# Kernel tuning notes

Hardware: AMD Instinct MI355X
Metric: run time of the kernel (lower is better)

Reference implementation:

```python
import jax, jax.numpy as jnp
import numpy as np

N, D, K = 16384, 256, 4096   # tokens, feature dim, codebook_size
GAMMA = 0.99


def setup_inputs() -> dict:
    key = jax.random.key(0)
    k1, k2, k3 = jax.random.split(key, 3)
    features = jax.random.normal(k1, (N, D), dtype=jnp.float32)
    mask = jax.random.uniform(k2, (N,)) < 0.9
    codebook = jax.random.normal(k3, (K, D), dtype=jnp.float32)  # hk RandomNormal init
    count = jnp.zeros((K,), jnp.float32)
    avg = jnp.zeros((K,), jnp.float32)
    return {"features": features, "mask": mask, "codebook": codebook,
            "count": count, "avg": avg}


def reference(features, mask, codebook, count, avg):
    sg = jax.lax.stop_gradient
    prev_codebook = codebook

    # pairwise squared distances [N, K] via ||f||^2 - 2 f.C^T + ||c||^2
    f2 = jnp.sum(features * features, axis=-1)            # [N]
    c2 = jnp.sum(codebook * codebook, axis=-1)            # [K]
    distance = f2[:, None] - 2.0 * (features @ codebook.T) + c2[None, :]
    distance = jnp.where(mask[:, None], distance, jnp.inf)

    assign_fwd = jnp.argmin(distance, axis=1)             # [N] nearest code per token
    assign_rev = jnp.argmin(distance, axis=0)             # [K] nearest token per code
    features_fwd = codebook[assign_fwd]                   # [N, D]
    features_rev = features[assign_rev]                   # [K, D]

    # straight-through estimator
    out_features = sg(features_fwd) + features - sg(features)

    total = jnp.maximum(mask.sum(), 1).astype(features.dtype)
    commitment = jnp.mean((sg(features_fwd) - features) ** 2, axis=-1)
    commitment_loss = jnp.where(mask, commitment, 0.0).sum() / total

    # scatter-add assignment counts (masked) and feature sums (unmasked, as in source)
    assignment_count = jnp.zeros((K,), jnp.float32).at[assign_fwd].add(
        mask.astype(jnp.float32))
    assignment_mask = assignment_count < 1

    count = (1.0 - GAMMA) * assignment_count + GAMMA * count
    avg = (1.0 - GAMMA) * assignment_count / total + GAMMA * avg
    alpha = jnp.exp(-avg * K * 10.0 / (1.0 - GAMMA) - 0.001)

    feat_sum = jnp.zeros_like(codebook).at[assign_fwd].add(features)  # [K, D]
    assigned_update = (GAMMA * codebook + (1.0 - GAMMA) * feat_sum)
    assigned_update = assigned_update / jnp.maximum(count[:, None], 1.0)
    unassigned_update = (1.0 - alpha)[:, None] * codebook + alpha[:, None] * features_rev
    new_codebook = jnp.where(assignment_mask[:, None], assigned_update, unassigned_update)

    # pmean(delta) is identity on a single device; final = prev + (prev - new), as in source
    codebook_delta = prev_codebook - new_codebook
    new_codebook = prev_codebook + codebook_delta

    unassigned_percent = (assignment_count > 0).mean()
    return (out_features, assign_fwd, commitment_loss, unassigned_percent,
            count, avg, new_codebook)
```

## Files before the change

kernel.cpp:

```cpp
#include <hip/hip_runtime.h>
#include <math.h>

typedef unsigned long long u64;
typedef unsigned int u32;

#define N_TOK 16384
#define DIM   256
#define KCB   4096

#define WS_ROWMIN   0
#define WS_COLMIN   131072
#define WS_CNT      163840
#define WS_CPART    180224
#define WS_TOTAL    181248
#define WS_FLAG     181252
#define WS_F2       181312
#define WS_C2       246848
#define WS_END      263232

#define OUT_FEAT    0
#define OUT_ASSIGN  4194304
#define OUT_CLOSS   4210688
#define OUT_UPCT    4210689
#define OUT_COUNT   4210690
#define OUT_AVG     4214786
#define OUT_CB      4218882

#define C_1MG 0.009999999776482582f

__device__ __forceinline__ u32 fkey(float d) {
    u32 u = __float_as_uint(d);
    return (u & 0x80000000u) ? ~u : (u | 0x80000000u);
}
__device__ __forceinline__ u64 u64min(u64 a, u64 b) { return a < b ? a : b; }
__device__ __forceinline__ u64 shflxor64(u64 v, int m) {
    int lo = __shfl_xor((int)(u32)(v & 0xFFFFFFFFULL), m, 64);
    int hi = __shfl_xor((int)(u32)(v >> 32), m, 64);
    return ((u64)(u32)hi << 32) | (u32)lo;
}
__device__ __forceinline__ bool read_mask(const void* mp, int flag, int n) {
    if (flag == 2) return ((const float*)mp)[n] != 0.0f;
    if (flag == 1) return ((const int*)mp)[n] != 0;
    return ((const unsigned char*)mp)[n] != 0;
}

__global__ void k_detect(const void* __restrict__ mp, int* __restrict__ flag) {
    if (threadIdx.x == 0) {
        const u32* w = (const u32*)mp;
        bool allf = true, alli = true, any1 = false;
        for (int i = 0; i < 64; ++i) {
            u32 x = w[i];
            if (x != 0u && x != 0x3F800000u) allf = false;
            if (x == 0x3F800000u) any1 = true;
            if (x > 1u) alli = false;
        }
        *flag = (allf && any1) ? 2 : (alli ? 1 : 0);
    }
}

__global__ __launch_bounds__(256)
void k_norms(const float* __restrict__ F, const float* __restrict__ CB,
             const void* __restrict__ mp, const int* __restrict__ flagp,
             float* __restrict__ f2, float* __restrict__ c2) {
    __shared__ float red[4];
    const int b = blockIdx.x, d = threadIdx.x;
    const float* src = (b < N_TOK) ? (F + (size_t)b * DIM) : (CB + (size_t)(b - N_TOK) * DIM);
    float v = src[d];
    float s = v * v;
#pragma unroll
    for (int m = 32; m > 0; m >>= 1) s += __shfl_xor(s, m, 64);
    if ((d & 63) == 0) red[d >> 6] = s;
    __syncthreads();
    if (d == 0) {
        float tot = red[0] + red[1] + red[2] + red[3];
        if (b < N_TOK) {
            bool msk = read_mask(mp, *flagp, b);
            f2[b] = msk ? tot : __builtin_huge_valf();
        } else {
            c2[b - N_TOK] = tot;
        }
    }
}

__global__ __launch_bounds__(256, 2)
void k_gemm(const float* __restrict__ F, const float* __restrict__ CB,
            const float* __restrict__ f2, const float* __restrict__ c2,
            u64* __restrict__ rowmin, u64* __restrict__ colmin) {
    __shared__ float As[128][32];
    __shared__ float Bs[128][32];
    __shared__ u64 colred[4][128];

    const int t = threadIdx.x;
    const int ty = t >> 4, tx = t & 15;
    const int wave = t >> 6;
    const int rowbase = blockIdx.x * 128;
    const int kseg = blockIdx.y * 512;

    u64 rowbest[8];
#pragma unroll
    for (int i = 0; i < 8; ++i) rowbest[i] = ~0ULL;

    for (int c = 0; c < 4; ++c) {
        const int kbase = kseg + c * 128;
        float acc[8][8];
#pragma unroll
        for (int i = 0; i < 8; ++i)
#pragma unroll
            for (int j = 0; j < 8; ++j) acc[i][j] = 0.0f;

        for (int dc = 0; dc < 8; ++dc) {
            const int db = dc * 32;
#pragma unroll
            for (int i = 0; i < 4; ++i) {
                int g = t + i * 256;
                int r = g >> 3;
                int d4 = (g & 7) << 2;
                int dsw = d4 ^ (((r >> 3) & 7) << 2);
                float4 va = *(const float4*)(F + (size_t)(rowbase + r) * DIM + db + d4);
                *(float4*)&As[r][dsw] = va;
                float4 vb = *(const float4*)(CB + (size_t)(kbase + r) * DIM + db + d4);
                *(float4*)&Bs[r][dsw] = vb;
            }
            __syncthreads();
#pragma unroll
            for (int dd = 0; dd < 32; dd += 4) {
                float4 a[8], b[8];
#pragma unroll
                for (int i = 0; i < 8; ++i)
                    a[i] = *(const float4*)&As[ty * 8 + i][dd ^ ((ty & 7) << 2)];
#pragma unroll
                for (int j = 0; j < 8; ++j)
                    b[j] = *(const float4*)&Bs[tx * 8 + j][dd ^ ((tx & 7) << 2)];
#pragma unroll
                for (int i = 0; i < 8; ++i)
#pragma unroll
                    for (int j = 0; j < 8; ++j) {
                        acc[i][j] = fmaf(a[i].x, b[j].x, acc[i][j]);
                        acc[i][j] = fmaf(a[i].y, b[j].y, acc[i][j]);
                        acc[i][j] = fmaf(a[i].z, b[j].z, acc[i][j]);
                        acc[i][j] = fmaf(a[i].w, b[j].w, acc[i][j]);
                    }
            }
            __syncthreads();
        }

        float c2k[8], f2r[8];
#pragma unroll
        for (int j = 0; j < 8; ++j) c2k[j] = c2[kbase + tx * 8 + j];
#pragma unroll
        for (int i = 0; i < 8; ++i) f2r[i] = f2[rowbase + ty * 8 + i];
        u64 cbst[8];
#pragma unroll
        for (int j = 0; j < 8; ++j) cbst[j] = ~0ULL;
#pragma unroll
        for (int i = 0; i < 8; ++i) {
#pragma unroll
            for (int j = 0; j < 8; ++j) {
                float dist = (f2r[i] - 2.0f * acc[i][j]) + c2k[j];
                u64 hk = (u64)fkey(dist) << 32;
                rowbest[i] = u64min(rowbest[i], hk | (u32)(kbase + tx * 8 + j));
                cbst[j]    = u64min(cbst[j],    hk | (u32)(rowbase + ty * 8 + i));
            }
        }
#pragma unroll
        for (int j = 0; j < 8; ++j) {
            cbst[j] = u64min(cbst[j], shflxor64(cbst[j], 16));
            cbst[j] = u64min(cbst[j], shflxor64(cbst[j], 32));
        }
        if ((t & 63) < 16) {
#pragma unroll
            for (int j = 0; j < 8; ++j) colred[wave][tx * 8 + j] = cbst[j];
        }
        __syncthreads();
        if (t < 128) {
            u64 m = u64min(u64min(colred[0][t], colred[1][t]),
                           u64min(colred[2][t], colred[3][t]));
            atomicMin(&colmin[kbase + t], m);
        }
        __syncthreads();
    }

#pragma unroll
    for (int i = 0; i < 8; ++i) {
        u64 r = rowbest[i];
        r = u64min(r, shflxor64(r, 1));
        r = u64min(r, shflxor64(r, 2));
        r = u64min(r, shflxor64(r, 4));
        r = u64min(r, shflxor64(r, 8));
        if (tx == 0) atomicMin(&rowmin[rowbase + ty * 8 + i], r);
    }
}

__global__ __launch_bounds__(256)
void k_token(const float* __restrict__ F, const float* __restrict__ CB,
             const u64* __restrict__ rowmin, const void* __restrict__ mp,
             const int* __restrict__ flagp,
             float* __restrict__ out_feat, float* __restrict__ out_assign,
             float* __restrict__ cnt, float* __restrict__ fsum,
             float* __restrict__ cpart) {
    __shared__ float red[4];
    const int n = blockIdx.x, d = threadIdx.x;
    const int k = (int)(u32)(rowmin[n] & 0xFFFFFFFFULL);
    const float f = F[(size_t)n * DIM + d];
    const float cv = CB[(size_t)k * DIM + d];
    out_feat[(size_t)n * DIM + d] = (cv + f) - f;
    const float df = cv - f;
    float s = df * df;
#pragma unroll
    for (int m = 32; m > 0; m >>= 1) s += __shfl_xor(s, m, 64);
    if ((d & 63) == 0) red[d >> 6] = s;
    __syncthreads();
    atomicAdd(&fsum[(size_t)k * DIM + d], f);
    if (d == 0) {
        out_assign[n] = (float)k;
        bool msk = read_mask(mp, *flagp, n);
        if (msk) {
            float tot = red[0] + red[1] + red[2] + red[3];
            atomicAdd(&cnt[k], 1.0f);
            atomicAdd(&cpart[n & 255], tot * (1.0f / 256.0f));
        }
    }
}

__global__ __launch_bounds__(256)
void k_scalars(const float* __restrict__ cnt, const float* __restrict__ cpart,
               float* __restrict__ totf, float* __restrict__ out) {
    __shared__ float redf[4], redc[4];
    __shared__ int redi[4];
    const int t = threadIdx.x;
    float ts = 0.0f;
    int asg = 0;
    for (int i = t; i < KCB; i += 256) {
        float v = cnt[i];
        ts += v;
        asg += (v > 0.0f) ? 1 : 0;
    }
    float cs = cpart[t];
#pragma unroll
    for (int m = 32; m > 0; m >>= 1) {
        ts += __shfl_xor(ts, m, 64);
        cs += __shfl_xor(cs, m, 64);
        asg += __shfl_xor(asg, m, 64);
    }
    if ((t & 63) == 0) { redf[t >> 6] = ts; redc[t >> 6] = cs; redi[t >> 6] = asg; }
    __syncthreads();
    if (t == 0) {
        float total = redf[0] + redf[1] + redf[2] + redf[3];
        total = fmaxf(total, 1.0f);
        float closs = (redc[0] + redc[1] + redc[2] + redc[3]) / total;
        int a = redi[0] + redi[1] + redi[2] + redi[3];
        totf[0] = total;
        out[OUT_CLOSS] = closs;
        out[OUT_UPCT] = (float)a / 4096.0f;
    }
}

__global__ __launch_bounds__(256)
void k_cbupd(const float* __restrict__ F, const float* __restrict__ CB,
             const float* __restrict__ cnt_in, const float* __restrict__ avg_in,
             const float* __restrict__ ac_, const float* __restrict__ fsum,
             const u64* __restrict__ colmin, const float* __restrict__ totf,
             float* __restrict__ out_count, float* __restrict__ out_avg,
             float* __restrict__ out_cb) {
    const int k = blockIdx.x, d = threadIdx.x;
    const float ac = ac_[k];
    const float total = totf[0];
    const float cn = C_1MG * ac + 0.99f * cnt_in[k];
    const float av = (C_1MG * ac) / total + 0.99f * avg_in[k];
    const float arg = ((-av * 4096.0f) * 10.0f) / C_1MG - 0.001f;
    const float alpha = expf(arg);
    const int tok = (int)(u32)(colmin[k] & 0xFFFFFFFFULL);
    const float cb = CB[(size_t)k * DIM + d];
    const float fs = fsum[(size_t)k * DIM + d];
    const float fr = F[(size_t)tok * DIM + d];
    const float assigned = (0.99f * cb + C_1MG * fs) / fmaxf(cn, 1.0f);
    const float unass = (1.0f - alpha) * cb + alpha * fr;
    const float nc = (ac < 1.0f) ? assigned : unass;
    out_cb[(size_t)k * DIM + d] = cb + (cb - nc);
    if (d == 0) { out_count[k] = cn; out_avg[k] = av; }
}

extern "C" void kernel_launch(void* const* d_in, const int* in_sizes, int n_in,
                              void* d_out, int out_size, void* d_ws, size_t ws_size,
                              hipStream_t stream) {
    const float* F   = (const float*)d_in[0];
    const void*  Mp  = d_in[1];
    const float* CB  = (const float*)d_in[2];
    const float* CNT = (const float*)d_in[3];
    const float* AVG = (const float*)d_in[4];
    float* out = (float*)d_out;
    char* ws = (char*)d_ws;
    if (ws_size < (size_t)WS_END) return;

    u64*   rowmin = (u64*)(ws + WS_ROWMIN);
    u64*   colmin = (u64*)(ws + WS_COLMIN);
    float* cnt    = (float*)(ws + WS_CNT);
    float* cpart  = (float*)(ws + WS_CPART);
    float* totf   = (float*)(ws + WS_TOTAL);
    int*   flag   = (int*)(ws + WS_FLAG);
    float* f2     = (float*)(ws + WS_F2);
    float* c2     = (float*)(ws + WS_C2);
    float* fsum   = out + OUT_CB;

    hipMemsetAsync(ws, 0xFF, 163840, stream);
    hipMemsetAsync(ws + WS_CNT, 0, WS_FLAG - WS_CNT, stream);
    hipMemsetAsync(fsum, 0, (size_t)KCB * DIM * sizeof(float), stream);

    k_detect<<<1, 64, 0, stream>>>(Mp, flag);
    k_norms<<<N_TOK + KCB, 256, 0, stream>>>(F, CB, Mp, flag, f2, c2);
    k_gemm<<<dim3(128, 8), 256, 0, stream>>>(F, CB, f2, c2, rowmin, colmin);
    k_token<<<N_TOK, 256, 0, stream>>>(F, CB, rowmin, Mp, flag,
                                       out + OUT_FEAT, out + OUT_ASSIGN,
                                       cnt, fsum, cpart);
    k_scalars<<<1, 256, 0, stream>>>(cnt, cpart, totf, out);
    k_cbupd<<<KCB, 256, 0, stream>>>(F, CB, CNT, AVG, cnt, fsum, colmin, totf,
                                     out + OUT_COUNT, out + OUT_AVG, out + OUT_CB);
}
```

Measured before the change: 641.6 us.

## Split distance GEMM into finer K tiles and raise occupancy target

The distance GEMM now gives each block a single 128-code tile instead of looping over four tiles, which quadruples the grid. The launch bound moves from 2 to 4 blocks per CU, and LDS operand reads shrink from float4 to float2 to lower register pressure. Per-row minima are reduced and pushed with atomics inside the row loop rather than kept live across chunks. This aims for more waves in flight to hide latency, at the cost of four times as many rowmin atomics and possible spills under the tighter register cap.

Result: no change. 639.5 us (-0.3%).

```diff
diff --git a/kernel.cpp b/kernel.cpp
--- a/kernel.cpp
+++ b/kernel.cpp
@@ -82,7 +82,7 @@
     }
 }
 
-__global__ __launch_bounds__(256, 2)
+__global__ __launch_bounds__(256, 4)
 void k_gemm(const float* __restrict__ F, const float* __restrict__ CB,
             const float* __restrict__ f2, const float* __restrict__ c2,
             u64* __restrict__ rowmin, u64* __restrict__ colmin) {
@@ -94,100 +94,86 @@
     const int ty = t >> 4, tx = t & 15;
     const int wave = t >> 6;
     const int rowbase = blockIdx.x * 128;
-    const int kseg = blockIdx.y * 512;
-
-    u64 rowbest[8];
-#pragma unroll
-    for (int i = 0; i < 8; ++i) rowbest[i] = ~0ULL;
-
-    for (int c = 0; c < 4; ++c) {
-        const int kbase = kseg + c * 128;
-        float acc[8][8];
-#pragma unroll
-        for (int i = 0; i < 8; ++i)
-#pragma unroll
-            for (int j = 0; j < 8; ++j) acc[i][j] = 0.0f;
-
-        for (int dc = 0; dc < 8; ++dc) {
-            const int db = dc * 32;
-#pragma unroll
-            for (int i = 0; i < 4; ++i) {
-                int g = t + i * 256;
-                int r = g >> 3;
-                int d4 = (g & 7) << 2;
-                int dsw = d4 ^ (((r >> 3) & 7) << 2);
-                float4 va = *(const float4*)(F + (size_t)(rowbase + r) * DIM + db + d4);
-                *(float4*)&As[r][dsw] = va;
-                float4 vb = *(const float4*)(CB + (size_t)(kbase + r) * DIM + db + d4);
-                *(float4*)&Bs[r][dsw] = vb;
-            }
-            __syncthreads();
-#pragma unroll
-            for (int dd = 0; dd < 32; dd += 4) {
-                float4 a[8], b[8];
-#pragma unroll
-                for (int i = 0; i < 8; ++i)
-                    a[i] = *(const float4*)&As[ty * 8 + i][dd ^ ((ty & 7) << 2)];
-#pragma unroll
-                for (int j = 0; j < 8; ++j)
-                    b[j] = *(const float4*)&Bs[tx * 8 + j][dd ^ ((tx & 7) << 2)];
-#pragma unroll
-                for (int i = 0; i < 8; ++i)
-#pragma unroll
-                    for (int j = 0; j < 8; ++j) {
-                        acc[i][j] = fmaf(a[i].x, b[j].x, acc[i][j]);
-                        acc[i][j] = fmaf(a[i].y, b[j].y, acc[i][j]);
-                        acc[i][j] = fmaf(a[i].z, b[j].z, acc[i][j]);
-                        acc[i][j] = fmaf(a[i].w, b[j].w, acc[i][j]);
-                    }
-            }
-            __syncthreads();
-        }
-
-        float c2k[8], f2r[8];
-#pragma unroll
-        for (int j = 0; j < 8; ++j) c2k[j] = c2[kbase + tx * 8 + j];
-#pragma unroll
-        for (int i = 0; i < 8; ++i) f2r[i] = f2[rowbase + ty * 8 + i];
-        u64 cbst[8];
-#pragma unroll
-        for (int j = 0; j < 8; ++j) cbst[j] = ~0ULL;
-#pragma unroll
-        for (int i = 0; i < 8; ++i) {
-#pragma unroll
-            for (int j = 0; j < 8; ++j) {
-                float dist = (f2r[i] - 2.0f * acc[i][j]) + c2k[j];
-                u64 hk = (u64)fkey(dist) << 32;
-                rowbest[i] = u64min(rowbest[i], hk | (u32)(kbase + tx * 8 + j));
-                cbst[j]    = u64min(cbst[j],    hk | (u32)(rowbase + ty * 8 + i));
-            }
-        }
+    const int kbase = blockIdx.y * 128;
+
+    float acc[8][8];
+#pragma unroll
+    for (int i = 0; i < 8; ++i)
+#pragma unroll
+        for (int j = 0; j < 8; ++j) acc[i][j] = 0.0f;
+
+    for (int dc = 0; dc < 8; ++dc) {
+        const int db = dc * 32;
+#pragma unroll
+        for (int i = 0; i < 4; ++i) {
+            int g = t + i * 256;
+            int r = g >> 3;
+            int c4 = (g & 7) << 2;
+            int sw = c4 ^ (((r >> 3) & 7) << 2);
+            *(float4*)&As[r][sw] = *(const float4*)(F + (size_t)(rowbase + r) * DIM + db + c4);
+            *(float4*)&Bs[r][sw] = *(const float4*)(CB + (size_t)(kbase + r) * DIM + db + c4);
+        }
+        __syncthreads();
+#pragma unroll
+        for (int dd = 0; dd < 32; dd += 2) {
+            float2 a[8], b[8];
+#pragma unroll
+            for (int i = 0; i < 8; ++i)
+                a[i] = *(const float2*)&As[ty * 8 + i][dd ^ ((ty & 7) << 2)];
+#pragma unroll
+            for (int j = 0; j < 8; ++j)
+                b[j] = *(const float2*)&Bs[tx * 8 + j][dd ^ ((tx & 7) << 2)];
+#pragma unroll
+            for (int i = 0; i < 8; ++i)
+#pragma unroll
+                for (int j = 0; j < 8; ++j) {
+                    acc[i][j] = fmaf(a[i].x, b[j].x, acc[i][j]);
+                    acc[i][j] = fmaf(a[i].y, b[j].y, acc[i][j]);
+                }
+        }
+        __syncthreads();
+    }
+
+    float c2k[8];
+#pragma unroll
+    for (int j = 0; j < 8; ++j) c2k[j] = c2[kbase + tx * 8 + j];
+    u64 cbst[8];
+#pragma unroll
+    for (int j = 0; j < 8; ++j) cbst[j] = ~0ULL;
+
+#pragma unroll
+    for (int i = 0; i < 8; ++i) {
+        const int row = rowbase + ty * 8 + i;
+        const float f2r = f2[row];
+        u64 rbst = ~0ULL;
 #pragma unroll
         for (int j = 0; j < 8; ++j) {
-            cbst[j] = u64min(cbst[j], shflxor64(cbst[j], 16));
-            cbst[j] = u64min(cbst[j], shflxor64(cbst[j], 32));
-        }
-        if ((t & 63) < 16) {
-#pragma unroll
-            for (int j = 0; j < 8; ++j) colred[wave][tx * 8 + j] = cbst[j];
-        }
-        __syncthreads();
-        if (t < 128) {
-            u64 m = u64min(u64min(colred[0][t], colred[1][t]),
-                           u64min(colred[2][t], colred[3][t]));
-            atomicMin(&colmin[kbase + t], m);
-        }
-        __syncthreads();
-    }
-
-#pragma unroll
-    for (int i = 0; i < 8; ++i) {
-        u64 r = rowbest[i];
-        r = u64min(r, shflxor64(r, 1));
-        r = u64min(r, shflxor64(r, 2));
-        r = u64min(r, shflxor64(r, 4));
-        r = u64min(r, shflxor64(r, 8));
-        if (tx == 0) atomicMin(&rowmin[rowbase + ty * 8 + i], r);
+            float dist = (f2r - 2.0f * acc[i][j]) + c2k[j];
+            u64 hk = (u64)fkey(dist) << 32;
+            rbst    = u64min(rbst, hk | (u32)(kbase + tx * 8 + j));
+            cbst[j] = u64min(cbst[j], hk | (u32)row);
+        }
+        rbst = u64min(rbst, shflxor64(rbst, 1));
+        rbst = u64min(rbst, shflxor64(rbst, 2));
+        rbst = u64min(rbst, shflxor64(rbst, 4));
+        rbst = u64min(rbst, shflxor64(rbst, 8));
+        if (tx == 0) atomicMin(&rowmin[row], rbst);
+    }
+
+#pragma unroll
+    for (int j = 0; j < 8; ++j) {
+        cbst[j] = u64min(cbst[j], shflxor64(cbst[j], 16));
+        cbst[j] = u64min(cbst[j], shflxor64(cbst[j], 32));
+    }
+    if ((t & 63) < 16) {
+#pragma unroll
+        for (int j = 0; j < 8; ++j) colred[wave][tx * 8 + j] = cbst[j];
+    }
+    __syncthreads();
+    if (t < 128) {
+        u64 m = u64min(u64min(colred[0][t], colred[1][t]),
+                       u64min(colred[2][t], colred[3][t]));
+        atomicMin(&colmin[kbase + t], m);
     }
 }
 
@@ -308,7 +294,7 @@
 
     k_detect<<<1, 64, 0, stream>>>(Mp, flag);
     k_norms<<<N_TOK + KCB, 256, 0, stream>>>(F, CB, Mp, flag, f2, c2);
-    k_gemm<<<dim3(128, 8), 256, 0, stream>>>(F, CB, f2, c2, rowmin, colmin);
+    k_gemm<<<dim3(128, 32), 256, 0, stream>>>(F, CB, f2, c2, rowmin, colmin);
     k_token<<<N_TOK, 256, 0, stream>>>(F, CB, rowmin, Mp, flag,
                                        out + OUT_FEAT, out + OUT_ASSIGN,
                                        cnt, fsum, cpart);
```
